# Optimization experiments

Hardware: AMD Instinct MI355X
Metric: run time of the kernel (lower is better)

The kernel has to match this reference:

```python
import jax, jax.numpy as jnp
import numpy as np

E, B, L, H1, H2, C = 8, 4096, 512, 1024, 512, 40


def setup_inputs() -> dict:
    key = jax.random.key(0)
    ks = jax.random.split(key, 9)
    return {
        "x_s": jax.random.normal(ks[0], (B, L), jnp.float32),
        "x_p": jax.random.normal(ks[1], (B, L), jnp.float32),
        "W1": jax.random.normal(ks[2], (E, 2 * L, H1), jnp.float32) / np.sqrt(2 * L).astype(np.float32),
        "b1": jax.random.normal(ks[3], (E, H1), jnp.float32) * 0.01,
        "W2": jax.random.normal(ks[4], (E, H1, H2), jnp.float32) / np.sqrt(H1).astype(np.float32),
        "b2": jax.random.normal(ks[5], (E, H2), jnp.float32) * 0.01,
        "W3": jax.random.normal(ks[6], (E, H2, C), jnp.float32) / np.sqrt(H2).astype(np.float32),
        "b3": jax.random.normal(ks[7], (E, C), jnp.float32) * 0.01,
        "sub_module_label": jax.random.randint(ks[8], (B,), 0, E, dtype=jnp.int32),
        "sub_id": 0,
    }


def reference(x_s, x_p, W1, b1, W2, b2, W3, b3, sub_module_label, sub_id):
    # Encoders (EEGNet/SCN/DCN) abstracted as identity: x_s / x_p are latent features.
    # Cls_HEAD.forward: x = cat([x_p, x_s], dim=1); per-sample routed 3-layer ELU MLP head.
    # Dropout is identity in eval mode.
    x = jnp.concatenate([x_p, x_s], axis=1)                      # [B, 2L]
    h = jax.nn.elu(jnp.einsum('bi,eih->ebh', x, W1) + b1[:, None, :])   # [E, B, H1]
    h = jax.nn.elu(jnp.einsum('ebh,ehk->ebk', h, W2) + b2[:, None, :])  # [E, B, H2]
    out_all = jnp.einsum('ebk,ekc->ebc', h, W3) + b3[:, None, :]        # [E, B, C]
    # select each sample's routed expert output
    bidx = jnp.arange(x.shape[0])
    return out_all[sub_module_label, bidx]                       # [B, C]
```

## Files before the change

### kernel.cpp

```cpp
#include <hip/hip_runtime.h>
#include <hip/hip_bf16.h>
#include <math.h>

#define En   8
#define Bn   4096
#define Ln   512
#define K1n  1024
#define H1n  1024
#define H2n  512
#define Cn   40
#define NP3  48

typedef unsigned short u16;
typedef __attribute__((ext_vector_type(8))) short bf16x8;
typedef __attribute__((ext_vector_type(4))) float f32x4;

__device__ __forceinline__ u16 f2b(float f) {
    union { float f; unsigned int u; } v; v.f = f;
    unsigned int r = v.u + 0x7FFF + ((v.u >> 16) & 1);
    return (u16)(r >> 16);
}

__device__ __forceinline__ void g2l16(const void* g, void* l) {
    __builtin_amdgcn_global_load_lds(
        (const __attribute__((address_space(1))) unsigned int*)(unsigned long long)g,
        (__attribute__((address_space(3))) unsigned int*)(unsigned int)(unsigned long long)l,
        16, 0, 0);
}

__device__ __forceinline__ void wtrans64(
    const float* __restrict__ Wsrc, u16* __restrict__ Wdst,
    int K, int N, int k0, int n0, int tid, float* sm )
{
    #pragma unroll
    for (int s = 0; s < 4; s++) {
        int idx = tid + s * 256;
        int kk = idx >> 4, c4 = (idx & 15) * 4;
        float4 v = *(const float4*)&Wsrc[(size_t)(k0 + kk) * N + n0 + c4];
        float* row = sm + kk * 65 + c4;
        row[0] = v.x; row[1] = v.y; row[2] = v.z; row[3] = v.w;
    }
    __syncthreads();
    #pragma unroll
    for (int s = 0; s < 4; s++) {
        int idx = tid + s * 256;
        int nn = idx >> 4, kc = (idx & 15) * 4;
        ushort4 o = make_ushort4(f2b(sm[(kc + 0) * 65 + nn]), f2b(sm[(kc + 1) * 65 + nn]),
                                 f2b(sm[(kc + 2) * 65 + nn]), f2b(sm[(kc + 3) * 65 + nn]));
        *(ushort4*)&Wdst[(size_t)(n0 + nn) * K + k0 + kc] = o;
    }
}

#define P1_TOT (1 + 256 + 2048)

__global__ __launch_bounds__(256) void prep1_kernel(
    const float* __restrict__ xs, const float* __restrict__ xp,
    const float* __restrict__ W1, const int* __restrict__ label,
    int* __restrict__ meta, int* __restrict__ perm,
    u16* __restrict__ Xb, u16* __restrict__ W1t)
{
    __shared__ __align__(16) float sm[64 * 65];
    const int bid = blockIdx.x;
    const int tid = threadIdx.x;

    if (bid == 0) {
        int* cnt = (int*)sm;
        int* off = cnt + En;
        if (tid < En) cnt[tid] = 0;
        __syncthreads();
        for (int b = tid; b < Bn; b += 256) atomicAdd(&cnt[label[b]], 1);
        __syncthreads();
        if (tid == 0) {
            int run = 0;
            for (int e = 0; e < En; e++) { off[e] = run; run += cnt[e]; }
            off[En] = run;
        }
        __syncthreads();
        if (tid < En) cnt[tid] = off[tid];
        __syncthreads();
        for (int b = tid; b < Bn; b += 256) {
            int e = label[b];
            perm[atomicAdd(&cnt[e], 1)] = b;
        }
        if (tid <= En) meta[tid] = off[tid];
    } else if (bid < 257) {
        int r0 = (bid - 1) * 16;
        #pragma unroll 4
        for (int s = 0; s < 16; s++) {
            int r = r0 + s;
            int k = tid * 4;
            const float* src = (k < Ln) ? (xp + (size_t)r * Ln + k)
                                        : (xs + (size_t)r * Ln + (k - Ln));
            float4 v = *(const float4*)src;
            *(ushort4*)&Xb[(size_t)r * K1n + k] =
                make_ushort4(f2b(v.x), f2b(v.y), f2b(v.z), f2b(v.w));
        }
    } else {
        int b = bid - 257;
        int e = b >> 8, rem = b & 255;
        int k0 = (rem >> 4) * 64, n0 = (rem & 15) * 64;
        wtrans64(W1 + (size_t)e * K1n * H1n, W1t + (size_t)e * H1n * K1n,
                 K1n, H1n, k0, n0, tid, sm);
    }
}

template <int K, int N, int TM, int TN, bool GATHER, bool FUSE3, bool PREP2>
__global__ __launch_bounds__(256) void mfma_gemm(
    const u16* __restrict__ A, const u16* __restrict__ Wt,
    const float* __restrict__ bias, const int* __restrict__ meta,
    const int* __restrict__ perm, u16* __restrict__ outb,
    const u16* __restrict__ Wt3, float* __restrict__ outf,
    const float* __restrict__ W2f, const float* __restrict__ W3f,
    const float* __restrict__ b3v, const int* __restrict__ labelv,
    u16* __restrict__ W2t_o, u16* __restrict__ W3t_o)
{
    constexpr int BK    = 32;
    constexpr int T     = K / BK;
    constexpr int NTC   = N / TN;
    constexpr int NTRk  = Bn / TM + En;
    constexpr int NGEMM = NTRk * NTC;
    constexpr int ASLOT = TM * 4;
    constexpr int BSLOT = TN * 4;
    constexpr int STAGE = ASLOT + BSLOT;
    constexpr int ALOAD = ASLOT / 256;
    constexpr int BLOAD = BSLOT / 256;
    constexpr int LW    = ALOAD + BLOAD;
    constexpr int HSTR  = TN + 8;
    constexpr int SMST  = 3 * STAGE * 8;
    constexpr int SMU16 = (FUSE3 && (TM * HSTR) > SMST) ? (TM * HSTR) : SMST;
    __shared__ __align__(16) u16 SM[SMU16];

    const int tid = threadIdx.x;
    const int bx = blockIdx.x;

    if (PREP2 && bx >= NGEMM) {
        int jb = bx - NGEMM;
        if (jb < 1024) {
            int e = jb >> 7, rem = jb & 127;
            int k0 = (rem >> 3) * 64, n0 = (rem & 7) * 64;
            wtrans64(W2f + (size_t)e * H1n * H2n, W2t_o + (size_t)e * H2n * H1n,
                     H1n, H2n, k0, n0, tid, (float*)SM);
        } else if (jb < 1024 + 128) {
            int b = jb - 1024;
            int e = b >> 4, k0 = (b & 15) * 32;
            const float* src = W3f + (size_t)e * H2n * Cn;
            u16* dst = W3t_o + (size_t)e * NP3 * H2n;
            float* t = (float*)SM;
            #pragma unroll
            for (int s = 0; s < 5; s++) {
                int idx = tid + s * 256;
                int kk = idx / Cn, nn = idx - kk * Cn;
                if (kk < 32) t[kk * 41 + nn] = src[(size_t)(k0 + kk) * Cn + nn];
            }
            __syncthreads();
            #pragma unroll
            for (int s = 0; s < 6; s++) {
                int idx = tid + s * 256;
                int nn = idx >> 5, kk = idx & 31;
                float v = (nn < Cn) ? t[kk * 41 + nn] : 0.f;
                dst[(size_t)nn * H2n + k0 + kk] = f2b(v);
            }
        } else {
            int b = jb - (1024 + 128);
            int r0 = b * 64;
            #pragma unroll
            for (int s = 0; s < 10; s++) {
                int idx = tid + s * 256;
                int r = r0 + idx / Cn;
                int c = idx - (idx / Cn) * Cn;
                outf[(size_t)r * Cn + c] = b3v[labelv[r] * Cn + c];
            }
        }
        return;
    }

    const int gx = (bx & 7) * (NGEMM / 8) + (bx >> 3);
    const int rt = gx % NTRk;
    const int col0 = (gx / NTRk) * TN;

    int expert = -1, row0 = 0, rowmax = 0, acc_t = 0;
    int prev = meta[0];
    #pragma unroll
    for (int e = 0; e < En; e++) {
        int nxt = meta[e + 1];
        int c = nxt - prev;
        int t = (c + TM - 1) / TM;
        if (expert < 0 && rt < acc_t + t) {
            expert = e; row0 = prev + (rt - acc_t) * TM; rowmax = nxt - 1;
        }
        acc_t += t; prev = nxt;
    }
    if (expert < 0) return;

    const u16* Wexp = Wt + (size_t)expert * N * K;

    const int lane = tid & 63;
    const int wid = tid >> 6;
    const int wm = (wid & 1) * (TM / 2);
    const int wn = (wid >> 1) * (TN / 2);
    const int l15 = lane & 15;
    const int lq = lane >> 4;

    const u16* aptr[ALOAD]; int aoff[ALOAD];
    const u16* bptr[BLOAD]; int boff[BLOAD];
    #pragma unroll
    for (int s = 0; s < ALOAD; s++) {
        int idx = tid + s * 256;
        int rl = idx >> 2, c = idx & 3;
        int kq = c ^ ((rl >> 1) & 3);
        int rg = row0 + rl; if (rg > rowmax) rg = rowmax;
        if (GATHER) rg = perm[rg];
        aptr[s] = A + (size_t)rg * K + kq * 8;
        aoff[s] = idx * 8;
    }
    #pragma unroll
    for (int s = 0; s < BLOAD; s++) {
        int idx = tid + s * 256;
        int rl = idx >> 2, c = idx & 3;
        int kq = c ^ ((rl >> 1) & 3);
        bptr[s] = Wexp + (size_t)(col0 + rl) * K + kq * 8;
        boff[s] = ASLOT * 8 + idx * 8;
    }

    constexpr int MI = TM / 32;
    constexpr int NJ = TN / 32;
    f32x4 acc[MI][NJ];
    #pragma unroll
    for (int i = 0; i < MI; i++)
        #pragma unroll
        for (int j = 0; j < NJ; j++) acc[i][j] = (f32x4){0.f, 0.f, 0.f, 0.f};

    const int cp = (lq ^ ((l15 >> 1) & 3)) * 8;

    auto stage_issue = [&](int buf, int t) {
        const int base = buf * (STAGE * 8);
        const int ko = t * BK;
        #pragma unroll
        for (int s = 0; s < ALOAD; s++) g2l16(aptr[s] + ko, &SM[base + aoff[s]]);
        #pragma unroll
        for (int s = 0; s < BLOAD; s++) g2l16(bptr[s] + ko, &SM[base + boff[s]]);
    };

    auto kstep = [&](int buf) {
        const u16* As = &SM[buf * (STAGE * 8)];
        const u16* Bs = As + ASLOT * 8;
        bf16x8 af[MI], bf[NJ];
        #pragma unroll
        for (int i = 0; i < MI; i++)
            af[i] = *(const bf16x8*)&As[(wm + i * 16 + l15) * BK + cp];
        #pragma unroll
        for (int j = 0; j < NJ; j++)
            bf[j] = *(const bf16x8*)&Bs[(wn + j * 16 + l15) * BK + cp];
        #pragma unroll
        for (int i = 0; i < MI; i++)
            #pragma unroll
            for (int j = 0; j < NJ; j++)
                acc[i][j] = __builtin_amdgcn_mfma_f32_16x16x32_bf16(
                    af[i], bf[j], acc[i][j], 0, 0, 0);
    };

    stage_issue(0, 0);
    asm volatile("" ::: "memory");
    stage_issue(1, 1);
    asm volatile("" ::: "memory");

    int rb = 0;
    for (int t = 0; t < T - 1; t++) {
        if constexpr (LW == 2)
            asm volatile("s_waitcnt vmcnt(2) lgkmcnt(0)" ::: "memory");
        else if constexpr (LW == 3)
            asm volatile("s_waitcnt vmcnt(3) lgkmcnt(0)" ::: "memory");
        else
            asm volatile("s_waitcnt vmcnt(4) lgkmcnt(0)" ::: "memory");
        __builtin_amdgcn_s_barrier();
        asm volatile("" ::: "memory");
        if (t + 2 < T) {
            int wb = rb + 2; if (wb >= 3) wb -= 3;
            stage_issue(wb, t + 2);
        }
        asm volatile("" ::: "memory");
        kstep(rb);
        rb = (rb == 2) ? 0 : rb + 1;
    }
    asm volatile("s_waitcnt vmcnt(0) lgkmcnt(0)" ::: "memory");
    __builtin_amdgcn_s_barrier();
    asm volatile("" ::: "memory");
    kstep(rb);

    if (!FUSE3) {
        #pragma unroll
        for (int i = 0; i < MI; i++) {
            #pragma unroll
            for (int j = 0; j < NJ; j++) {
                int col = col0 + wn + j * 16 + l15;
                float bv = bias[expert * N + col];
                #pragma unroll
                for (int r = 0; r < 4; r++) {
                    int grow = row0 + wm + i * 16 + lq * 4 + r;
                    if (grow <= rowmax) {
                        float v = acc[i][j][r] + bv;
                        v = (v > 0.f) ? v : (expf(v) - 1.f);
                        outb[(size_t)grow * N + col] = f2b(v);
                    }
                }
            }
        }
    } else {
        __syncthreads();
        u16* H = &SM[0];
        #pragma unroll
        for (int i = 0; i < MI; i++) {
            #pragma unroll
            for (int j = 0; j < NJ; j++) {
                int col = wn + j * 16 + l15;
                float bv = bias[expert * N + col0 + col];
                #pragma unroll
                for (int r = 0; r < 4; r++) {
                    float v = acc[i][j][r] + bv;
                    v = (v > 0.f) ? v : (expf(v) - 1.f);
                    H[(wm + i * 16 + lq * 4 + r) * HSTR + col] = f2b(v);
                }
            }
        }
        __syncthreads();
        constexpr int RI = TM / 64;
        constexpr int KC = TN / 32;
        const int rh = wid * (TM / 4);
        f32x4 a3[RI][3];
        #pragma unroll
        for (int ri = 0; ri < RI; ri++)
            #pragma unroll
            for (int j = 0; j < 3; j++) a3[ri][j] = (f32x4){0.f, 0.f, 0.f, 0.f};
        #pragma unroll
        for (int ki = 0; ki < KC; ki++) {
            bf16x8 ha[RI];
            #pragma unroll
            for (int ri = 0; ri < RI; ri++)
                ha[ri] = *(const bf16x8*)&H[(rh + ri * 16 + l15) * HSTR + ki * 32 + lq * 8];
            #pragma unroll
            for (int j = 0; j < 3; j++) {
                bf16x8 wb = *(const bf16x8*)
                    &Wt3[((size_t)expert * NP3 + j * 16 + l15) * H2n + col0 + ki * 32 + lq * 8];
                #pragma unroll
                for (int ri = 0; ri < RI; ri++)
                    a3[ri][j] = __builtin_amdgcn_mfma_f32_16x16x32_bf16(
                        ha[ri], wb, a3[ri][j], 0, 0, 0);
            }
        }
        #pragma unroll
        for (int j = 0; j < 3; j++) {
            int col = j * 16 + l15;
            if (col < Cn) {
                #pragma unroll
                for (int ri = 0; ri < RI; ri++) {
                    #pragma unroll
                    for (int r = 0; r < 4; r++) {
                        int grow = row0 + rh + ri * 16 + lq * 4 + r;
                        if (grow <= rowmax)
                            atomicAdd(&outf[(size_t)perm[grow] * Cn + col], a3[ri][j][r]);
                    }
                }
            }
        }
    }
}

extern "C" void kernel_launch(void* const* d_in, const int* in_sizes, int n_in,
                              void* d_out, int out_size, void* d_ws, size_t ws_size,
                              hipStream_t stream)
{
    const float* xs = (const float*)d_in[0];
    const float* xp = (const float*)d_in[1];
    const float* W1 = (const float*)d_in[2];
    const float* b1 = (const float*)d_in[3];
    const float* W2 = (const float*)d_in[4];
    const float* b2 = (const float*)d_in[5];
    const float* W3 = (const float*)d_in[6];
    const float* b3 = (const float*)d_in[7];
    const int* label = (const int*)d_in[8];
    float* out = (float*)d_out;

    char* ws = (char*)d_ws;
    int* meta = (int*)ws;
    int* perm = (int*)(ws + 64);
    u16* Xb  = (u16*)(ws + (64 << 10));
    u16* W1t = (u16*)(ws + (64 << 10) + (8  << 20));
    u16* W2t = (u16*)(ws + (64 << 10) + (24 << 20));
    u16* h1b = (u16*)(ws + (64 << 10) + (32 << 20));
    u16* W3t = (u16*)(ws + (64 << 10) + (40 << 20));

    prep1_kernel<<<P1_TOT, 256, 0, stream>>>(
        xs, xp, W1, label, meta, perm, Xb, W1t);

    mfma_gemm<K1n, H1n, 128, 64, true, false, true><<<640 + 1216, 256, 0, stream>>>(
        Xb, W1t, b1, meta, perm, h1b, nullptr, out,
        W2, W3, b3, label, W2t, W3t);

    mfma_gemm<H1n, H2n, 64, 64, false, true, false><<<576, 256, 0, stream>>>(
        h1b, W2t, b2, meta, perm, nullptr, W3t, out,
        nullptr, nullptr, nullptr, nullptr, nullptr, nullptr);
}
```

Before: 171.3 us.

## Move W2/W3 prep into prep kernel and deepen GEMM pipeline to four stages

Moves the W2 and W3 transpose/convert work and the bias-based output initialisation out of the first GEMM launch and into a single preparation kernel. The first GEMM now launches only its compute blocks. Both GEMMs also move from a three-buffer to a four-buffer LDS cp.async pipeline, issuing three stages ahead, with adjusted waitcnt values and an extra drain step. This is meant to hide more global-load latency, at the cost of more LDS per block, which may lower occupancy. The prep work also no longer overlaps with the first GEMM.

```diff
diff --git a/kernel.cpp b/kernel.cpp
--- a/kernel.cpp
+++ b/kernel.cpp
@@ -51,13 +51,16 @@
     }
 }
 
-#define P1_TOT (1 + 256 + 2048)
-
-__global__ __launch_bounds__(256) void prep1_kernel(
+#define PA_TOT 3521
+
+__global__ __launch_bounds__(256) void prep_all(
     const float* __restrict__ xs, const float* __restrict__ xp,
-    const float* __restrict__ W1, const int* __restrict__ label,
+    const float* __restrict__ W1, const float* __restrict__ W2,
+    const float* __restrict__ W3, const float* __restrict__ b3,
+    const int* __restrict__ label,
     int* __restrict__ meta, int* __restrict__ perm,
-    u16* __restrict__ Xb, u16* __restrict__ W1t)
+    u16* __restrict__ Xb, u16* __restrict__ W1t, u16* __restrict__ W2t,
+    u16* __restrict__ W3t, float* __restrict__ outf)
 {
     __shared__ __align__(16) float sm[64 * 65];
     const int bid = blockIdx.x;
@@ -95,24 +98,54 @@
             *(ushort4*)&Xb[(size_t)r * K1n + k] =
                 make_ushort4(f2b(v.x), f2b(v.y), f2b(v.z), f2b(v.w));
         }
-    } else {
+    } else if (bid < 2305) {
         int b = bid - 257;
         int e = b >> 8, rem = b & 255;
-        int k0 = (rem >> 4) * 64, n0 = (rem & 15) * 64;
         wtrans64(W1 + (size_t)e * K1n * H1n, W1t + (size_t)e * H1n * K1n,
-                 K1n, H1n, k0, n0, tid, sm);
-    }
-}
-
-template <int K, int N, int TM, int TN, bool GATHER, bool FUSE3, bool PREP2>
+                 K1n, H1n, (rem >> 4) * 64, (rem & 15) * 64, tid, sm);
+    } else if (bid < 3329) {
+        int b = bid - 2305;
+        int e = b >> 7, rem = b & 127;
+        wtrans64(W2 + (size_t)e * H1n * H2n, W2t + (size_t)e * H2n * H1n,
+                 H1n, H2n, (rem >> 3) * 64, (rem & 7) * 64, tid, sm);
+    } else if (bid < 3457) {
+        int b = bid - 3329;
+        int e = b >> 4, k0 = (b & 15) * 32;
+        const float* src = W3 + (size_t)e * H2n * Cn;
+        u16* dst = W3t + (size_t)e * NP3 * H2n;
+        float* t = sm;
+        #pragma unroll
+        for (int q = 0; q < 5; q++) {
+            int idx = tid + q * 256;
+            int kk = idx / Cn, nn = idx - kk * Cn;
+            if (kk < 32) t[kk * 41 + nn] = src[(size_t)(k0 + kk) * Cn + nn];
+        }
+        __syncthreads();
+        #pragma unroll
+        for (int q = 0; q < 6; q++) {
+            int idx = tid + q * 256;
+            int nn = idx >> 5, kk = idx & 31;
+            float v = (nn < Cn) ? t[kk * 41 + nn] : 0.f;
+            dst[(size_t)nn * H2n + k0 + kk] = f2b(v);
+        }
+    } else {
+        int r0 = (bid - 3457) * 64;
+        #pragma unroll
+        for (int s = 0; s < 10; s++) {
+            int idx = tid + s * 256;
+            int r = r0 + idx / Cn;
+            int c = idx - (idx / Cn) * Cn;
+            outf[(size_t)r * Cn + c] = b3[label[r] * Cn + c];
+        }
+    }
+}
+
+template <int K, int N, int TM, int TN, bool GATHER, bool FUSE3>
 __global__ __launch_bounds__(256) void mfma_gemm(
     const u16* __restrict__ A, const u16* __restrict__ Wt,
     const float* __restrict__ bias, const int* __restrict__ meta,
     const int* __restrict__ perm, u16* __restrict__ outb,
-    const u16* __restrict__ Wt3, float* __restrict__ outf,
-    const float* __restrict__ W2f, const float* __restrict__ W3f,
-    const float* __restrict__ b3v, const int* __restrict__ labelv,
-    u16* __restrict__ W2t_o, u16* __restrict__ W3t_o)
+    const u16* __restrict__ Wt3, float* __restrict__ outf)
 {
     constexpr int BK    = 32;
     constexpr int T     = K / BK;
@@ -126,53 +159,12 @@
     constexpr int BLOAD = BSLOT / 256;
     constexpr int LW    = ALOAD + BLOAD;
     constexpr int HSTR  = TN + 8;
-    constexpr int SMST  = 3 * STAGE * 8;
+    constexpr int SMST  = 4 * STAGE * 8;
     constexpr int SMU16 = (FUSE3 && (TM * HSTR) > SMST) ? (TM * HSTR) : SMST;
     __shared__ __align__(16) u16 SM[SMU16];
 
     const int tid = threadIdx.x;
     const int bx = blockIdx.x;
-
-    if (PREP2 && bx >= NGEMM) {
-        int jb = bx - NGEMM;
-        if (jb < 1024) {
-            int e = jb >> 7, rem = jb & 127;
-            int k0 = (rem >> 3) * 64, n0 = (rem & 7) * 64;
-            wtrans64(W2f + (size_t)e * H1n * H2n, W2t_o + (size_t)e * H2n * H1n,
-                     H1n, H2n, k0, n0, tid, (float*)SM);
-        } else if (jb < 1024 + 128) {
-            int b = jb - 1024;
-            int e = b >> 4, k0 = (b & 15) * 32;
-            const float* src = W3f + (size_t)e * H2n * Cn;
-            u16* dst = W3t_o + (size_t)e * NP3 * H2n;
-            float* t = (float*)SM;
-            #pragma unroll
-            for (int s = 0; s < 5; s++) {
-                int idx = tid + s * 256;
-                int kk = idx / Cn, nn = idx - kk * Cn;
-                if (kk < 32) t[kk * 41 + nn] = src[(size_t)(k0 + kk) * Cn + nn];
-            }
-            __syncthreads();
-            #pragma unroll
-            for (int s = 0; s < 6; s++) {
-                int idx = tid + s * 256;
-                int nn = idx >> 5, kk = idx & 31;
-                float v = (nn < Cn) ? t[kk * 41 + nn] : 0.f;
-                dst[(size_t)nn * H2n + k0 + kk] = f2b(v);
-            }
-        } else {
-            int b = jb - (1024 + 128);
-            int r0 = b * 64;
-            #pragma unroll
-            for (int s = 0; s < 10; s++) {
-                int idx = tid + s * 256;
-                int r = r0 + idx / Cn;
-                int c = idx - (idx / Cn) * Cn;
-                outf[(size_t)r * Cn + c] = b3v[labelv[r] * Cn + c];
-            }
-        }
-        return;
-    }
 
     const int gx = (bx & 7) * (NGEMM / 8) + (bx >> 3);
     const int rt = gx % NTRk;
@@ -240,7 +232,6 @@
         #pragma unroll
         for (int s = 0; s < BLOAD; s++) g2l16(bptr[s] + ko, &SM[base + boff[s]]);
     };
-
     auto kstep = [&](int buf) {
         const u16* As = &SM[buf * (STAGE * 8)];
         const u16* Bs = As + ASLOT * 8;
@@ -263,25 +254,30 @@
     asm volatile("" ::: "memory");
     stage_issue(1, 1);
     asm volatile("" ::: "memory");
+    stage_issue(2, 2);
+    asm volatile("" ::: "memory");
 
     int rb = 0;
-    for (int t = 0; t < T - 1; t++) {
+    for (int t = 0; t < T - 2; t++) {
         if constexpr (LW == 2)
-            asm volatile("s_waitcnt vmcnt(2) lgkmcnt(0)" ::: "memory");
-        else if constexpr (LW == 3)
-            asm volatile("s_waitcnt vmcnt(3) lgkmcnt(0)" ::: "memory");
+            asm volatile("s_waitcnt vmcnt(4) lgkmcnt(0)" ::: "memory");
         else
-            asm volatile("s_waitcnt vmcnt(4) lgkmcnt(0)" ::: "memory");
+            asm volatile("s_waitcnt vmcnt(6) lgkmcnt(0)" ::: "memory");
         __builtin_amdgcn_s_barrier();
         asm volatile("" ::: "memory");
-        if (t + 2 < T) {
-            int wb = rb + 2; if (wb >= 3) wb -= 3;
-            stage_issue(wb, t + 2);
-        }
+        if (t + 3 < T) stage_issue((rb + 3) & 3, t + 3);
         asm volatile("" ::: "memory");
         kstep(rb);
-        rb = (rb == 2) ? 0 : rb + 1;
-    }
+        rb = (rb + 1) & 3;
+    }
+    if constexpr (LW == 2)
+        asm volatile("s_waitcnt vmcnt(2) lgkmcnt(0)" ::: "memory");
+    else
+        asm volatile("s_waitcnt vmcnt(3) lgkmcnt(0)" ::: "memory");
+    __builtin_amdgcn_s_barrier();
+    asm volatile("" ::: "memory");
+    kstep(rb);
+    rb = (rb + 1) & 3;
     asm volatile("s_waitcnt vmcnt(0) lgkmcnt(0)" ::: "memory");
     __builtin_amdgcn_s_barrier();
     asm volatile("" ::: "memory");
@@ -389,14 +385,12 @@
     u16* h1b = (u16*)(ws + (64 << 10) + (32 << 20));
     u16* W3t = (u16*)(ws + (64 << 10) + (40 << 20));
 
-    prep1_kernel<<<P1_TOT, 256, 0, stream>>>(
-        xs, xp, W1, label, meta, perm, Xb, W1t);
-
-    mfma_gemm<K1n, H1n, 128, 64, true, false, true><<<640 + 1216, 256, 0, stream>>>(
-        Xb, W1t, b1, meta, perm, h1b, nullptr, out,
-        W2, W3, b3, label, W2t, W3t);
-
-    mfma_gemm<H1n, H2n, 64, 64, false, true, false><<<576, 256, 0, stream>>>(
-        h1b, W2t, b2, meta, perm, nullptr, W3t, out,
-        nullptr, nullptr, nullptr, nullptr, nullptr, nullptr);
-}
+    prep_all<<<PA_TOT, 256, 0, stream>>>(
+        xs, xp, W1, W2, W3, b3, label, meta, perm, Xb, W1t, W2t, W3t, out);
+
+    mfma_gemm<K1n, H1n, 128, 64, true, false><<<640, 256, 0, stream>>>(
+        Xb, W1t, b1, meta, perm, h1b, nullptr, out);
+
+    mfma_gemm<H1n, H2n, 64, 64, false, true><<<576, 256, 0, stream>>>(
+        h1b, W2t, b2, meta, perm, nullptr, W3t, out);
+}
```

New measurement: 169.9 us. About the same (-0.8%).
